# Kernel tuning notes

Hardware: AMD Instinct MI355X
Metric: run time of the kernel (lower is better)

The kernel has to match this reference:

```python
import jax, jax.numpy as jnp
import numpy as np

VOCAB, EMB, B, L, H, OUT = 100000, 300, 2048, 200, 128, 20

def setup_inputs() -> dict:
    key = jax.random.key(0)
    ks = jax.random.split(key, 7)
    x = jax.random.randint(ks[0], (B, L), 0, VOCAB, dtype=jnp.int64 if jax.config.read('jax_enable_x64') else jnp.int32)
    lengths = jax.random.randint(ks[1], (B,), 1, L + 1, dtype=x.dtype)  # avoid zero length
    emb_table = jax.random.normal(ks[2], (VOCAB, EMB), dtype=jnp.float32)
    W1 = jax.random.normal(ks[3], (EMB, H), dtype=jnp.float32) * (1.0 / np.sqrt(EMB))
    b1 = jax.random.normal(ks[4], (H,), dtype=jnp.float32) * 0.01
    W2 = jax.random.normal(ks[5], (H, OUT), dtype=jnp.float32) * (1.0 / np.sqrt(H))
    b2 = jax.random.normal(ks[6], (OUT,), dtype=jnp.float32) * 0.01
    return {"x": x, "lengths": lengths, "emb_table": emb_table,
            "W1": W1, "b1": b1, "W2": W2, "b2": b2}

def reference(x, lengths, emb_table, W1, b1, W2, b2):
    # embedding lookup: [B, L, EMB]
    emb = emb_table[x]
    # faithful to original: sum over FULL sequence, divide by per-sample length
    rep = emb.sum(axis=1) / lengths.astype(emb.dtype)[:, None]  # [B, EMB]
    h = jax.nn.relu(rep @ W1 + b1)                              # [B, H]
    logits = h @ W2 + b2                                        # [B, OUT]
    return logits
```

## Files before the change

### kernel.cpp

```cpp
#include <hip/hip_runtime.h>

typedef _Float16 f16;
typedef _Float16 f16x8 __attribute__((ext_vector_type(8)));
typedef float    f32x4 __attribute__((ext_vector_type(4)));

#define VOCAB 100000
#define BB   2048
#define LL   200
#define EMB  300
#define HH   128
#define OUTD 20
#define RPW  50
#define KPAD 320

__global__ void w1t_prep(const float* __restrict__ W1,
                         f16* __restrict__ w1t_hi,
                         f16* __restrict__ w1t_lo)
{
    const int n = blockIdx.x;
    const int k = threadIdx.x;
    const float v = (k < EMB) ? W1[(size_t)k * HH + n] : 0.f;
    const f16 hi = (f16)v;
    const f16 lo = (f16)(v - (float)hi);
    w1t_hi[(size_t)n * KPAD + k] = hi;
    w1t_lo[(size_t)n * KPAD + k] = lo;
}

#define BMv7 64
#define NBLK ((VOCAB + BMv7 - 1) / BMv7)

#define AFI(mt, ks, l) ((((mt) * 10 + (ks)) * 64 + (l)) * 8)
#define BFI(hl, nt, l) ((((hl) * 8 + (nt)) * 64 + (l)) * 8)

__global__ __launch_bounds__(256, 2) void proj_mfma(
    const float* __restrict__ table,
    const f16*   __restrict__ w1t_hi,
    const f16*   __restrict__ w1t_lo,
    f16*         __restrict__ P)
{
    __shared__ f16 Af[4 * 10 * 64 * 8];
    __shared__ f16 Bf[2 * 8 * 64 * 8];

    const int t    = threadIdx.x;
    const int w    = t >> 6;
    const int lane = t & 63;
    const int row0 = blockIdx.x * BMv7;

    const int kg   = lane >> 4;
    const int arow = row0 + w * 16 + (lane & 15);
    const bool aok = (arow < VOCAB);
    const float* ap = table + (size_t)arow * EMB + kg * 8;

    float4 sa[10][2];
    #pragma unroll
    for (int i = 0; i < 10; ++i) {
        const int k = 32 * i + 8 * kg;
        const float4 z = make_float4(0.f, 0.f, 0.f, 0.f);
        sa[i][0] = (aok && k + 4 <= EMB) ? *(const float4*)(ap + 32 * i)     : z;
        sa[i][1] = (aok && k + 8 <= EMB) ? *(const float4*)(ap + 32 * i + 4) : z;
    }

    const int bn   = t >> 1;
    const int bkg0 = (t & 1) * 2;
    const f16* bh_src = w1t_hi + (size_t)bn * KPAD + bkg0 * 8;
    const f16* bl_src = w1t_lo + (size_t)bn * KPAD + bkg0 * 8;
    const int bnt = bn >> 4;
    const int bl0 = (bkg0 << 4) | (bn & 15);
    const int bl1 = ((bkg0 + 1) << 4) | (bn & 15);

    f16x8 rbh0 = *(const f16x8*)(bh_src);
    f16x8 rbh1 = *(const f16x8*)(bh_src + 8);
    f16x8 rbl0 = *(const f16x8*)(bl_src);
    f16x8 rbl1 = *(const f16x8*)(bl_src + 8);

    #pragma unroll
    for (int i = 0; i < 10; ++i) {
        const float v[8] = {sa[i][0].x, sa[i][0].y, sa[i][0].z, sa[i][0].w,
                            sa[i][1].x, sa[i][1].y, sa[i][1].z, sa[i][1].w};
        f16x8 h;
        #pragma unroll
        for (int j = 0; j < 8; ++j) h[j] = (f16)v[j];
        *(f16x8*)&Af[AFI(w, i, lane)] = h;
    }
    *(f16x8*)&Bf[BFI(0, bnt, bl0)] = rbh0;
    *(f16x8*)&Bf[BFI(0, bnt, bl1)] = rbh1;
    *(f16x8*)&Bf[BFI(1, bnt, bl0)] = rbl0;
    *(f16x8*)&Bf[BFI(1, bnt, bl1)] = rbl1;
    __syncthreads();

    f32x4 acc[4][2];
    #pragma unroll
    for (int i = 0; i < 4; ++i)
        #pragma unroll
        for (int j = 0; j < 2; ++j) acc[i][j] = (f32x4)0.f;

    const int ntb = 2 * w;

    for (int ks = 0; ks < 10; ++ks) {
        if (ks + 1 < 10) {
            const int ko = (ks + 1) * 32;
            rbh0 = *(const f16x8*)(bh_src + ko);
            rbh1 = *(const f16x8*)(bh_src + ko + 8);
            rbl0 = *(const f16x8*)(bl_src + ko);
            rbl1 = *(const f16x8*)(bl_src + ko + 8);
        }

        f16x8 a[4];
        #pragma unroll
        for (int m4 = 0; m4 < 4; ++m4)
            a[m4] = *(const f16x8*)&Af[AFI(m4, ks, lane)];
        f16x8 bh[2], bl[2];
        #pragma unroll
        for (int n2 = 0; n2 < 2; ++n2) {
            bh[n2] = *(const f16x8*)&Bf[BFI(0, ntb + n2, lane)];
            bl[n2] = *(const f16x8*)&Bf[BFI(1, ntb + n2, lane)];
        }

        #pragma unroll
        for (int n2 = 0; n2 < 2; ++n2)
            #pragma unroll
            for (int m4 = 0; m4 < 4; ++m4) {
                acc[m4][n2] = __builtin_amdgcn_mfma_f32_16x16x32_f16(a[m4], bh[n2], acc[m4][n2], 0, 0, 0);
                acc[m4][n2] = __builtin_amdgcn_mfma_f32_16x16x32_f16(a[m4], bl[n2], acc[m4][n2], 0, 0, 0);
            }

        __syncthreads();
        if (ks + 1 < 10) {
            *(f16x8*)&Bf[BFI(0, bnt, bl0)] = rbh0;
            *(f16x8*)&Bf[BFI(0, bnt, bl1)] = rbh1;
            *(f16x8*)&Bf[BFI(1, bnt, bl0)] = rbl0;
            *(f16x8*)&Bf[BFI(1, bnt, bl1)] = rbl1;
            __syncthreads();
        }
    }

    #pragma unroll
    for (int m4 = 0; m4 < 4; ++m4) {
        const int rb = row0 + m4 * 16 + 4 * (lane >> 4);
        #pragma unroll
        for (int n2 = 0; n2 < 2; ++n2) {
            const int col = (ntb + n2) * 16 + (lane & 15);
            const f32x4 v = acc[m4][n2];
            #pragma unroll
            for (int j = 0; j < 4; ++j) {
                const int row = rb + j;
                if (row < VOCAB)
                    P[(size_t)row * HH + col] = (f16)v[j];
            }
        }
    }
}

__global__ __launch_bounds__(256) void gather_mlp(
    const int*   __restrict__ x,
    const int*   __restrict__ lengths,
    const f16*   __restrict__ P,
    const float* __restrict__ b1,
    const float* __restrict__ W2,
    const float* __restrict__ b2,
    float*       __restrict__ out)
{
    __shared__ float part_s[16][HH];
    __shared__ float h_s[HH];

    const int b    = blockIdx.x;
    const int t    = threadIdx.x;
    const int lane = t & 63;
    const int w    = t >> 6;

    const int myidx = (lane < RPW) ? x[b * LL + RPW * w + lane] : 0;

    const int c = lane & 15;
    const size_t coff = (size_t)c * 8;

    int rid[13];
    #pragma unroll
    for (int i = 0; i < 12; ++i) {
        const int r0 = __builtin_amdgcn_readlane(myidx, 4 * i + 0);
        const int r1 = __builtin_amdgcn_readlane(myidx, 4 * i + 1);
        const int r2 = __builtin_amdgcn_readlane(myidx, 4 * i + 2);
        const int r3 = __builtin_amdgcn_readlane(myidx, 4 * i + 3);
        const int rlo = (lane & 16) ? r1 : r0;
        const int rhi = (lane & 16) ? r3 : r2;
        rid[i] = (lane & 32) ? rhi : rlo;
    }
    {
        const int r0 = __builtin_amdgcn_readlane(myidx, 48);
        const int r1 = __builtin_amdgcn_readlane(myidx, 49);
        rid[12] = (lane & 16) ? r1 : r0;
    }

    f16x8 vb[13];
    #pragma unroll
    for (int i = 0; i < 13; ++i)
        vb[i] = *(const f16x8*)(P + (size_t)rid[i] * HH + coff);

    float acc[8];
    #pragma unroll
    for (int j = 0; j < 8; ++j) acc[j] = 0.f;
    #pragma unroll
    for (int i = 0; i < 12; ++i)
        #pragma unroll
        for (int j = 0; j < 8; ++j) acc[j] += (float)vb[i][j];
    if (lane < 32) {
        #pragma unroll
        for (int j = 0; j < 8; ++j) acc[j] += (float)vb[12][j];
    }

    *(float4*)&part_s[t >> 4][c * 8]     = make_float4(acc[0], acc[1], acc[2], acc[3]);
    *(float4*)&part_s[t >> 4][c * 8 + 4] = make_float4(acc[4], acc[5], acc[6], acc[7]);
    __syncthreads();

    const float inv_len = 1.0f / (float)lengths[b];
    if (t < HH) {
        float s = 0.f;
        #pragma unroll
        for (int p = 0; p < 16; ++p) s += part_s[p][t];
        h_s[t] = fmaxf(fmaf(s, inv_len, b1[t]), 0.f);
    }
    __syncthreads();

    if (t < OUTD) {
        float o = b2[t];
        #pragma unroll
        for (int k = 0; k < HH; ++k)
            o = fmaf(h_s[k], W2[k * OUTD + t], o);
        out[b * OUTD + t] = o;
    }
}

#define NSRT 256
__global__ __launch_bounds__(256) void fused_dnn(
    const int*   __restrict__ x,
    const int*   __restrict__ lengths,
    const float* __restrict__ table,
    const float* __restrict__ W1,
    const float* __restrict__ b1,
    const float* __restrict__ W2,
    const float* __restrict__ b2,
    float*       __restrict__ out)
{
    __shared__ int    idx_s[NSRT];
    __shared__ float4 part_s[4][76];
    __shared__ float  rep_s[EMB];
    __shared__ float  h_part[2][HH];
    __shared__ float  h_s[HH];

    const int b    = blockIdx.x;
    const int t    = threadIdx.x;
    const int w    = t >> 6;
    const int lane = t & 63;

    idx_s[t] = (t < LL) ? x[b * LL + t] : 0x7FFFFFFF;
    __syncthreads();

    #pragma unroll
    for (int k = 2; k <= NSRT; k <<= 1) {
        #pragma unroll
        for (int j = k >> 1; j > 0; j >>= 1) {
            const int ixj = t ^ j;
            if (ixj > t) {
                const int a0 = idx_s[t];
                const int a1 = idx_s[ixj];
                const bool up = ((t & k) == 0);
                if ((a0 > a1) == up) { idx_s[t] = a1; idx_s[ixj] = a0; }
            }
            __syncthreads();
        }
    }

    const int myidx = (lane < RPW) ? idx_s[w + 4 * lane] : 0;

    float4 acc_a = make_float4(0.f, 0.f, 0.f, 0.f);
    float4 acc_b = make_float4(0.f, 0.f, 0.f, 0.f);
    const bool hasb = (lane < (EMB / 4 - 64));

    #pragma unroll 5
    for (int i = 0; i < RPW; ++i) {
        const int ridx = __builtin_amdgcn_readlane(myidx, i);
        const float4* row = (const float4*)(table + (size_t)ridx * EMB);
        float4 va = row[lane];
        acc_a.x += va.x; acc_a.y += va.y; acc_a.z += va.z; acc_a.w += va.w;
        if (hasb) {
            float4 vb = row[64 + lane];
            acc_b.x += vb.x; acc_b.y += vb.y; acc_b.z += vb.z; acc_b.w += vb.w;
        }
    }

    part_s[w][lane] = acc_a;
    if (hasb) part_s[w][64 + lane] = acc_b;
    __syncthreads();

    const float inv_len = 1.0f / (float)lengths[b];
    const float* ps = (const float*)part_s;
    {
        float s = ps[t] + ps[304 + t] + ps[608 + t] + ps[912 + t];
        rep_s[t] = s * inv_len;
    }
    if (t < (EMB - 256)) {
        int c = 256 + t;
        float s = ps[c] + ps[304 + c] + ps[608 + c] + ps[912 + c];
        rep_s[c] = s * inv_len;
    }
    __syncthreads();

    {
        const int half = t >> 7;
        const int col  = t & 127;
        float hacc = (half == 0) ? b1[col] : 0.0f;
        const int k0 = half * (EMB / 2);
        #pragma unroll 5
        for (int k = k0; k < k0 + EMB / 2; ++k)
            hacc = fmaf(rep_s[k], W1[k * HH + col], hacc);
        h_part[half][col] = hacc;
    }
    __syncthreads();
    if (t < HH)
        h_s[t] = fmaxf(h_part[0][t] + h_part[1][t], 0.0f);
    __syncthreads();

    if (t < OUTD) {
        float oacc = b2[t];
        #pragma unroll
        for (int k = 0; k < HH; ++k)
            oacc = fmaf(h_s[k], W2[k * OUTD + t], oacc);
        out[b * OUTD + t] = oacc;
    }
}

extern "C" void kernel_launch(void* const* d_in, const int* in_sizes, int n_in,
                              void* d_out, int out_size, void* d_ws, size_t ws_size,
                              hipStream_t stream) {
    const int*   x       = (const int*)  d_in[0];
    const int*   lengths = (const int*)  d_in[1];
    const float* table   = (const float*)d_in[2];
    const float* W1      = (const float*)d_in[3];
    const float* b1      = (const float*)d_in[4];
    const float* W2      = (const float*)d_in[5];
    const float* b2      = (const float*)d_in[6];
    float*       out     = (float*)d_out;

    const size_t PELEMS   = (size_t)VOCAB * HH;
    const size_t W1TELEMS = (size_t)HH * KPAD;
    const size_t NEED = (PELEMS + 2 * W1TELEMS) * sizeof(f16);

    if (d_ws != nullptr && ws_size >= NEED) {
        f16* P      = (f16*)d_ws;
        f16* w1t_hi = P + PELEMS;
        f16* w1t_lo = w1t_hi + W1TELEMS;
        w1t_prep<<<HH, KPAD, 0, stream>>>(W1, w1t_hi, w1t_lo);
        proj_mfma<<<NBLK, 256, 0, stream>>>(table, w1t_hi, w1t_lo, P);
        gather_mlp<<<BB, 256, 0, stream>>>(x, lengths, P, b1, W2, b2, out);
    } else {
        fused_dnn<<<BB, 256, 0, stream>>>(x, lengths, table, W1, b1, W2, b2, out);
    }
}
```

Measured before the change: 246.3 us.

## Pre-swizzle W1 into MFMA fragment layout and stage output through LDS

The W1 prep kernel now writes hi/lo halves directly in the per-lane MFMA B-fragment order, so proj_mfma loads B fragments straight from global memory into registers. This removes the shared-memory B buffer and the two block barriers per k-step. The LDS footprint shrinks, so launch bounds are raised to allow 4 blocks per CU. Output tiles are staged in padded LDS and written as coalesced 16-byte row stores instead of scattered 2-byte stores. The cost is that each wave re-reads W1 fragments from global/L2 instead of sharing them through LDS.

New measurement: 234.0 us. 1.05x faster.

```diff
diff --git a/kernel.cpp b/kernel.cpp
--- a/kernel.cpp
+++ b/kernel.cpp
@@ -13,38 +13,43 @@
 #define RPW  50
 #define KPAD 320
 
-__global__ void w1t_prep(const float* __restrict__ W1,
-                         f16* __restrict__ w1t_hi,
-                         f16* __restrict__ w1t_lo)
+#define FGI(hl, nt, ks, l, j) (((((hl) * 8 + (nt)) * 10 + (ks)) * 64 + (l)) * 8 + (j))
+#define W1F_ELEMS (2 * 8 * 10 * 64 * 8)
+
+__global__ void w1f_prep(const float* __restrict__ W1,
+                         f16* __restrict__ w1f)
 {
     const int n = blockIdx.x;
     const int k = threadIdx.x;
     const float v = (k < EMB) ? W1[(size_t)k * HH + n] : 0.f;
     const f16 hi = (f16)v;
     const f16 lo = (f16)(v - (float)hi);
-    w1t_hi[(size_t)n * KPAD + k] = hi;
-    w1t_lo[(size_t)n * KPAD + k] = lo;
-}
-
-#define BMv7 64
-#define NBLK ((VOCAB + BMv7 - 1) / BMv7)
+    const int nt = n >> 4;
+    const int ks = k >> 5;
+    const int kk = k & 31;
+    const int lane = ((kk >> 3) << 4) | (n & 15);
+    const int j = kk & 7;
+    w1f[FGI(0, nt, ks, lane, j)] = hi;
+    w1f[FGI(1, nt, ks, lane, j)] = lo;
+}
+
+#define BMv8 64
+#define NBLK ((VOCAB + BMv8 - 1) / BMv8)
 
 #define AFI(mt, ks, l) ((((mt) * 10 + (ks)) * 64 + (l)) * 8)
-#define BFI(hl, nt, l) ((((hl) * 8 + (nt)) * 64 + (l)) * 8)
-
-__global__ __launch_bounds__(256, 2) void proj_mfma(
+#define PSW 136
+
+__global__ __launch_bounds__(256, 4) void proj_mfma(
     const float* __restrict__ table,
-    const f16*   __restrict__ w1t_hi,
-    const f16*   __restrict__ w1t_lo,
+    const f16*   __restrict__ w1f,
     f16*         __restrict__ P)
 {
-    __shared__ f16 Af[4 * 10 * 64 * 8];
-    __shared__ f16 Bf[2 * 8 * 64 * 8];
+    alignas(16) __shared__ f16 Af[4 * 10 * 64 * 8];
 
     const int t    = threadIdx.x;
     const int w    = t >> 6;
     const int lane = t & 63;
-    const int row0 = blockIdx.x * BMv7;
+    const int row0 = blockIdx.x * BMv8;
 
     const int kg   = lane >> 4;
     const int arow = row0 + w * 16 + (lane & 15);
@@ -59,20 +64,6 @@
         sa[i][0] = (aok && k + 4 <= EMB) ? *(const float4*)(ap + 32 * i)     : z;
         sa[i][1] = (aok && k + 8 <= EMB) ? *(const float4*)(ap + 32 * i + 4) : z;
     }
-
-    const int bn   = t >> 1;
-    const int bkg0 = (t & 1) * 2;
-    const f16* bh_src = w1t_hi + (size_t)bn * KPAD + bkg0 * 8;
-    const f16* bl_src = w1t_lo + (size_t)bn * KPAD + bkg0 * 8;
-    const int bnt = bn >> 4;
-    const int bl0 = (bkg0 << 4) | (bn & 15);
-    const int bl1 = ((bkg0 + 1) << 4) | (bn & 15);
-
-    f16x8 rbh0 = *(const f16x8*)(bh_src);
-    f16x8 rbh1 = *(const f16x8*)(bh_src + 8);
-    f16x8 rbl0 = *(const f16x8*)(bl_src);
-    f16x8 rbl1 = *(const f16x8*)(bl_src + 8);
-
     #pragma unroll
     for (int i = 0; i < 10; ++i) {
         const float v[8] = {sa[i][0].x, sa[i][0].y, sa[i][0].z, sa[i][0].w,
@@ -82,10 +73,6 @@
         for (int j = 0; j < 8; ++j) h[j] = (f16)v[j];
         *(f16x8*)&Af[AFI(w, i, lane)] = h;
     }
-    *(f16x8*)&Bf[BFI(0, bnt, bl0)] = rbh0;
-    *(f16x8*)&Bf[BFI(0, bnt, bl1)] = rbh1;
-    *(f16x8*)&Bf[BFI(1, bnt, bl0)] = rbl0;
-    *(f16x8*)&Bf[BFI(1, bnt, bl1)] = rbl1;
     __syncthreads();
 
     f32x4 acc[4][2];
@@ -96,57 +83,68 @@
 
     const int ntb = 2 * w;
 
+    const f16* bh0p = w1f + FGI(0, ntb,     0, lane, 0);
+    const f16* bh1p = w1f + FGI(0, ntb + 1, 0, lane, 0);
+    const f16* bl0p = w1f + FGI(1, ntb,     0, lane, 0);
+    const f16* bl1p = w1f + FGI(1, ntb + 1, 0, lane, 0);
+    const int KSTRIDE = 64 * 8;
+
+    f16x8 cb0 = *(const f16x8*)(bh0p);
+    f16x8 cb1 = *(const f16x8*)(bh1p);
+    f16x8 cb2 = *(const f16x8*)(bl0p);
+    f16x8 cb3 = *(const f16x8*)(bl1p);
+
     for (int ks = 0; ks < 10; ++ks) {
+        f16x8 nb0, nb1, nb2, nb3;
         if (ks + 1 < 10) {
-            const int ko = (ks + 1) * 32;
-            rbh0 = *(const f16x8*)(bh_src + ko);
-            rbh1 = *(const f16x8*)(bh_src + ko + 8);
-            rbl0 = *(const f16x8*)(bl_src + ko);
-            rbl1 = *(const f16x8*)(bl_src + ko + 8);
+            const int o = (ks + 1) * KSTRIDE;
+            nb0 = *(const f16x8*)(bh0p + o);
+            nb1 = *(const f16x8*)(bh1p + o);
+            nb2 = *(const f16x8*)(bl0p + o);
+            nb3 = *(const f16x8*)(bl1p + o);
         }
 
         f16x8 a[4];
         #pragma unroll
         for (int m4 = 0; m4 < 4; ++m4)
             a[m4] = *(const f16x8*)&Af[AFI(m4, ks, lane)];
-        f16x8 bh[2], bl[2];
-        #pragma unroll
-        for (int n2 = 0; n2 < 2; ++n2) {
-            bh[n2] = *(const f16x8*)&Bf[BFI(0, ntb + n2, lane)];
-            bl[n2] = *(const f16x8*)&Bf[BFI(1, ntb + n2, lane)];
-        }
-
-        #pragma unroll
-        for (int n2 = 0; n2 < 2; ++n2)
-            #pragma unroll
-            for (int m4 = 0; m4 < 4; ++m4) {
-                acc[m4][n2] = __builtin_amdgcn_mfma_f32_16x16x32_f16(a[m4], bh[n2], acc[m4][n2], 0, 0, 0);
-                acc[m4][n2] = __builtin_amdgcn_mfma_f32_16x16x32_f16(a[m4], bl[n2], acc[m4][n2], 0, 0, 0);
-            }
-
-        __syncthreads();
-        if (ks + 1 < 10) {
-            *(f16x8*)&Bf[BFI(0, bnt, bl0)] = rbh0;
-            *(f16x8*)&Bf[BFI(0, bnt, bl1)] = rbh1;
-            *(f16x8*)&Bf[BFI(1, bnt, bl0)] = rbl0;
-            *(f16x8*)&Bf[BFI(1, bnt, bl1)] = rbl1;
-            __syncthreads();
-        }
-    }
-
+
+        #pragma unroll
+        for (int m4 = 0; m4 < 4; ++m4) {
+            acc[m4][0] = __builtin_amdgcn_mfma_f32_16x16x32_f16(a[m4], cb0, acc[m4][0], 0, 0, 0);
+            acc[m4][0] = __builtin_amdgcn_mfma_f32_16x16x32_f16(a[m4], cb2, acc[m4][0], 0, 0, 0);
+            acc[m4][1] = __builtin_amdgcn_mfma_f32_16x16x32_f16(a[m4], cb1, acc[m4][1], 0, 0, 0);
+            acc[m4][1] = __builtin_amdgcn_mfma_f32_16x16x32_f16(a[m4], cb3, acc[m4][1], 0, 0, 0);
+        }
+        cb0 = nb0; cb1 = nb1; cb2 = nb2; cb3 = nb3;
+    }
+
+    __syncthreads();
+    f16* Ps = Af;
     #pragma unroll
     for (int m4 = 0; m4 < 4; ++m4) {
-        const int rb = row0 + m4 * 16 + 4 * (lane >> 4);
+        const int rb = m4 * 16 + 4 * (lane >> 4);
         #pragma unroll
         for (int n2 = 0; n2 < 2; ++n2) {
             const int col = (ntb + n2) * 16 + (lane & 15);
             const f32x4 v = acc[m4][n2];
             #pragma unroll
-            for (int j = 0; j < 4; ++j) {
-                const int row = rb + j;
-                if (row < VOCAB)
-                    P[(size_t)row * HH + col] = (f16)v[j];
-            }
+            for (int j = 0; j < 4; ++j)
+                Ps[(rb + j) * PSW + col] = (f16)v[j];
+        }
+    }
+    __syncthreads();
+
+    {
+        const int srow = t >> 2;
+        const int sc   = (t & 3) * 32;
+        const int grow = row0 + srow;
+        if (grow < VOCAB) {
+            f16* dst = P + (size_t)grow * HH + sc;
+            const f16* src = Ps + srow * PSW + sc;
+            #pragma unroll
+            for (int m = 0; m < 4; ++m)
+                *(f16x8*)(dst + 8 * m) = *(const f16x8*)(src + 8 * m);
         }
     }
 }
@@ -340,16 +338,14 @@
     const float* b2      = (const float*)d_in[6];
     float*       out     = (float*)d_out;
 
-    const size_t PELEMS   = (size_t)VOCAB * HH;
-    const size_t W1TELEMS = (size_t)HH * KPAD;
-    const size_t NEED = (PELEMS + 2 * W1TELEMS) * sizeof(f16);
+    const size_t PELEMS = (size_t)VOCAB * HH;
+    const size_t NEED   = (PELEMS + W1F_ELEMS) * sizeof(f16);
 
     if (d_ws != nullptr && ws_size >= NEED) {
-        f16* P      = (f16*)d_ws;
-        f16* w1t_hi = P + PELEMS;
-        f16* w1t_lo = w1t_hi + W1TELEMS;
-        w1t_prep<<<HH, KPAD, 0, stream>>>(W1, w1t_hi, w1t_lo);
-        proj_mfma<<<NBLK, 256, 0, stream>>>(table, w1t_hi, w1t_lo, P);
+        f16* P   = (f16*)d_ws;
+        f16* w1f = P + PELEMS;
+        w1f_prep<<<HH, KPAD, 0, stream>>>(W1, w1f);
+        proj_mfma<<<NBLK, 256, 0, stream>>>(table, w1f, P);
         gather_mlp<<<BB, 256, 0, stream>>>(x, lengths, P, b1, W2, b2, out);
     } else {
         fused_dnn<<<BB, 256, 0, stream>>>(x, lengths, table, W1, b1, W2, b2, out);
```
